# Performance work log

Measured on AMD Instinct MI355X. Metric: run time of the kernel, lower is better.

## Reference

```python
import jax, jax.numpy as jnp
import numpy as np

E = 65536          # number of edges (cell pairs)
D = 256            # hidden_dim
P = 8              # n_lr_pairs


def setup_inputs() -> dict:
    key = jax.random.key(0)
    k1, k2, k3, k4, k5, k6, k7 = jax.random.split(key, 7)
    scale = 1.0 / np.sqrt(D)
    z_src = jax.random.normal(k1, (E, D), dtype=jnp.float32)
    z_dst = jax.random.normal(k2, (E, D), dtype=jnp.float32)
    lr_pair_idx = jax.random.randint(k3, (E,), 0, P, dtype=jnp.int64)
    # Per-LR-pair Linear(D, D): y = x @ W.T + b  (torch convention, W: [out, in])
    W_lr = jax.random.normal(k4, (P, D, D), dtype=jnp.float32) * scale
    b_lr = jax.random.normal(k5, (P, D), dtype=jnp.float32) * scale
    # nn.Bilinear(D, D, 1): weight [1, D, D], bias [1]
    W_bil = jax.random.normal(k6, (1, D, D), dtype=jnp.float32) * scale
    b_bil = jax.random.normal(k7, (1,), dtype=jnp.float32) * scale
    return {"z_src": z_src, "z_dst": z_dst, "W_lr": W_lr, "b_lr": b_lr,
            "W_bil": W_bil, "b_bil": b_bil, "lr_pair_idx": lr_pair_idx}


def _forward(z_src, z_dst, W_lr, b_lr, W_bil, b_bil, lr_pair_idx):
    # Per-LR-pair linear projection of z_src (MoE-style routing).
    # Fixed small loop over P experts; each iteration is a dense GEMM over
    # all E edges, masked to the edges routed to that pair. All idx values
    # lie in [0, P), so the zeros-init in the original is fully overwritten.
    z_proj = jnp.zeros_like(z_src)
    for p in range(P):
        mask = (lr_pair_idx == p)[:, None]                      # [E, 1]
        y_p = z_src @ W_lr[p].T + b_lr[p]                       # [E, D]
        z_proj = jnp.where(mask, y_p, z_proj)
    # Bilinear scoring: score_e = z_proj_e @ W_bil[0] @ z_dst_e + b_bil
    t = z_proj @ W_bil[0]                                       # [E, D]
    scores = jnp.sum(t * z_dst, axis=-1, keepdims=True) + b_bil  # [E, 1]
    return scores


def reference(z_src, z_dst, W_lr, b_lr, W_bil, b_bil, lr_pair_idx):
    return _forward(z_src, z_dst, W_lr, b_lr, W_bil, b_bil, lr_pair_idx)
```

## Files before the change

### kernel.cpp

```cpp
#include <hip/hip_runtime.h>
#include <hip/hip_bf16.h>
#include <cstddef>

#define NE 65536
#define ND 256
#define NP 8
#define SB 32
#define NSB (NE / SB)
#define TR 32

typedef short bf16x8 __attribute__((ext_vector_type(8)));
typedef float f32x4  __attribute__((ext_vector_type(4)));

__device__ __forceinline__ unsigned short f2bf(float f) {
  unsigned int u = __float_as_uint(f);
  u += 0x7FFFu + ((u >> 16) & 1u);
  return (unsigned short)(u >> 16);
}
__device__ __forceinline__ float bf2f(unsigned short h) {
  return __uint_as_float(((unsigned int)h) << 16);
}
__device__ __forceinline__ int load_idx(const void* idxraw, int is32, int e) {
  return is32 ? ((const int*)idxraw)[e] : (int)((const long long*)idxraw)[e];
}
__device__ __forceinline__ int sniff_is32(const void* idxraw, int* lflag) {
  int tid = threadIdx.x;
  if (tid == 0) *lflag = 0;
  __syncthreads();
  const unsigned int* w = (const unsigned int*)idxraw;
  unsigned int val = w[(((int)blockIdx.x & 63) * 256 + (tid & 255)) * 2 + 1];
  if (__any(val != 0) && (tid & 63) == 0) atomicOr(lflag, 1);
  __syncthreads();
  return *lflag;
}

__global__ __launch_bounds__(256) void k_pre0(const float* __restrict__ Wbil,
                                              const float* __restrict__ blr,
                                              const void* __restrict__ idxraw,
                                              unsigned short* __restrict__ WbT,
                                              float* __restrict__ v,
                                              int* __restrict__ counts) {
  int b = blockIdx.x, t = threadIdx.x;
  if (b < 32) {
    int s = b * 256 + t;
    int kt = s >> 10, c = (s >> 6) & 15, l = s & 63;
    int col = c * 16 + (l & 15);
    int k0 = kt * 32 + (l >> 4) * 8;
    union { uint4 u; unsigned short h[8]; } uu;
#pragma unroll
    for (int j = 0; j < 8; ++j)
      uu.h[j] = f2bf(Wbil[(k0 + j) * ND + col]);
    *(uint4*)(WbT + (size_t)s * 8) = uu.u;
  } else if (b < 40) {
    int p = b - 32;
    float s = 0.f;
    for (int k = 0; k < ND; ++k)
      s = fmaf(blr[p * ND + k], Wbil[k * ND + t], s);
    v[p * ND + t] = s;
  } else {
    __shared__ int lflag;
    int is32 = sniff_is32(idxraw, &lflag);
    int hb = b - 40;
    int w = t >> 6, l = t & 63;
    int e = hb * 256 + w * 64 + l;
    int p = load_idx(idxraw, is32, e);
    int sb0 = hb * 8 + w * 2;
#pragma unroll
    for (int q = 0; q < NP; ++q) {
      unsigned long long m = __ballot(p == q);
      if (l == q)      counts[q * NSB + sb0]     = __popcll(m & 0xFFFFFFFFull);
      if (l == 32 + q) counts[q * NSB + sb0 + 1] = __popcll(m >> 32);
    }
  }
}

__global__ __launch_bounds__(256) void k_scan(const int* __restrict__ counts,
                                              int* __restrict__ hdr,
                                              int* __restrict__ bases) {
  __shared__ int part[NP][32], cpre[NP][32], cnt[NP], shoff[NP];
  int t = threadIdx.x;
  int q = t >> 5, i = t & 31;
  int s = 0;
  for (int j = 0; j < 64; ++j) s += counts[q * NSB + i * 64 + j];
  part[q][i] = s;
  __syncthreads();
  if (t < NP) {
    int run = 0;
    for (int k = 0; k < 32; ++k) { cpre[t][k] = run; run += part[t][k]; }
    cnt[t] = run;
  }
  __syncthreads();
  if (t == 0) {
    int o = 0, tt = 0;
    for (int p = 0; p < NP; ++p) {
      shoff[p] = o; hdr[p] = o; hdr[9 + p] = tt;
      o += cnt[p];
      tt += (cnt[p] + TR - 1) / TR;
    }
    hdr[NP] = o; hdr[9 + NP] = tt;
  }
  __syncthreads();
  int run = shoff[q] + cpre[q][i];
  for (int j = 0; j < 64; ++j) {
    int sb = i * 64 + j;
    bases[q * NSB + sb] = run;
    run += counts[q * NSB + sb];
  }
}

__global__ __launch_bounds__(256) void k_cpre(const float* __restrict__ Wlr,
                                              const unsigned short* __restrict__ WbT,
                                              unsigned short* __restrict__ Cst) {
  __shared__ unsigned short aF[2048 * 8];
  int blk = blockIdx.x;
  int p = blk >> 2;
  int i0 = (blk & 3) * 64;
  int tid = threadIdx.x;
  const float* Wp = Wlr + (size_t)p * ND * ND;
#pragma unroll
  for (int it = 0; it < 8; ++it) {
    int s = tid + it * 256;
    int kt = s >> 8, r = (s >> 6) & 3, l = s & 63;
    int i = r * 16 + (l & 15);
    int k0 = kt * 32 + (l >> 4) * 8;
    union { uint4 u; unsigned short h[8]; } uu;
#pragma unroll
    for (int j = 0; j < 8; ++j)
      uu.h[j] = f2bf(Wp[(size_t)(k0 + j) * ND + i0 + i]);
    *(uint4*)(aF + (size_t)s * 8) = uu.u;
  }
  __syncthreads();
  int w = tid >> 6, l = tid & 63;
  f32x4 zero = {0.f, 0.f, 0.f, 0.f};
  f32x4 acc[16];
#pragma unroll
  for (int c = 0; c < 16; ++c) acc[c] = zero;
  for (int kt = 0; kt < 8; ++kt) {
    bf16x8 a = *(const bf16x8*)(aF + (size_t)((kt * 4 + w) * 64 + l) * 8);
#pragma unroll
    for (int c = 0; c < 16; ++c) {
      bf16x8 bb = *(const bf16x8*)(WbT + (size_t)((kt * 16 + c) * 64 + l) * 8);
      acc[c] = __builtin_amdgcn_mfma_f32_16x16x32_bf16(a, bb, acc[c], 0, 0, 0);
    }
  }
  unsigned short* Cp = Cst + (size_t)p * ND * ND;
#pragma unroll
  for (int c = 0; c < 16; ++c) {
#pragma unroll
    for (int q = 0; q < 4; ++q) {
      int i = i0 + w * 16 + ((l >> 4) * 4) + q;
      int j = c * 16 + (l & 15);
      int pos = ((i >> 5) * 16 + (j >> 4)) * 512 + (((i >> 3) & 3) * 16 + (j & 15)) * 8 + (i & 7);
      Cp[pos] = f2bf(acc[c][q]);
    }
  }
}

__global__ __launch_bounds__(64) void k_perm(const void* __restrict__ idxraw,
                                             const int* __restrict__ bases,
                                             int* __restrict__ perm) {
  __shared__ int lflag;
  int l = threadIdx.x;
  int b = blockIdx.x;
  if (l == 0) lflag = 0;
  __syncthreads();
  {
    const unsigned int* w = (const unsigned int*)idxraw;
    unsigned int val = w[((b & 63) * 64 + l) * 2 + 1];
    if (__any(val != 0) && l == 0) atomicOr(&lflag, 1);
  }
  __syncthreads();
  int is32 = lflag;
  int base = b * SB;
  int p = (l < SB) ? load_idx(idxraw, is32, base + l) : 999;
  unsigned long long lt = (l == 63) ? (~0ull >> 1) : ((1ull << l) - 1ull);
  int rank = 0, gq = 0;
#pragma unroll
  for (int q = 0; q < NP; ++q) {
    unsigned long long m = __ballot(p == q);
    if (p == q) { rank = __popcll(m & lt); gq = q; }
  }
  if (l < SB) perm[bases[gq * NSB + b] + rank] = base + l;
}

__global__ __launch_bounds__(512, 8) void k_main(const float* __restrict__ zsrc,
                                                 const float* __restrict__ zdst,
                                                 const int* __restrict__ perm,
                                                 const int* __restrict__ hdr,
                                                 const unsigned short* __restrict__ Cst,
                                                 const float* __restrict__ v,
                                                 const float* __restrict__ bbil,
                                                 float* __restrict__ out) {
  __shared__ unsigned short zs[8192];
  __shared__ unsigned short zd[8192];
  __shared__ float red[8][TR];
  __shared__ int eids[TR];
  __shared__ int shdr[18];
  int tid = threadIdx.x;
  if (tid < 18) shdr[tid] = hdr[tid];
  __syncthreads();
  int bid = blockIdx.x;
  int g = bid >> 3, r = bid & 7;
  int p = g & 7;
  int t = ((g >> 3) << 3) + r;
  int cnt = shdr[p + 1] - shdr[p];
  if (t * TR >= cnt) return;
  int ebase = shdr[p] + t * TR;
  int nrow = cnt - t * TR; if (nrow > TR) nrow = TR;
  if (tid < TR) eids[tid] = perm[ebase + (tid < nrow ? tid : nrow - 1)];
  __syncthreads();
  int w = tid >> 6, l = tid & 63;
  int kt0 = l >> 3, q0 = (l >> 1) & 3, par0 = l & 1;
#pragma unroll
  for (int i = 0; i < 4; ++i) {
    int row = w * 4 + i;
    int e = eids[row];
    float4 fs = *(const float4*)(zsrc + (size_t)e * ND + l * 4);
    float4 fd = *(const float4*)(zdst + (size_t)e * ND + l * 4);
    union { unsigned long long u; unsigned short h[4]; } us, ud;
    us.h[0] = f2bf(fs.x); us.h[1] = f2bf(fs.y); us.h[2] = f2bf(fs.z); us.h[3] = f2bf(fs.w);
    ud.h[0] = f2bf(fd.x); ud.h[1] = f2bf(fd.y); ud.h[2] = f2bf(fd.z); ud.h[3] = f2bf(fd.w);
    unsigned gg = (unsigned)((kt0 * 2 + (row >> 4)) * 64 + (row & 15) + 16 * q0);
    gg ^= ((gg >> 6) & 7u) << 1;
    *(unsigned long long*)((char*)zs + gg * 16 + par0 * 8) = us.u;
    *(unsigned long long*)((char*)zd + ((unsigned)(row * 512 + l * 8) ^ (((unsigned)row & 7u) << 5))) = ud.u;
  }
  __syncthreads();
  const unsigned short* Cp = Cst + (size_t)p * ND * ND;
  f32x4 zero = {0.f, 0.f, 0.f, 0.f};
  f32x4 acc[2][2];
#pragma unroll
  for (int sr = 0; sr < 2; ++sr)
#pragma unroll
    for (int cl = 0; cl < 2; ++cl) acc[sr][cl] = zero;
  int hh = l >> 4, rr = l & 15;
#pragma unroll
  for (int kt = 0; kt < 8; ++kt) {
    bf16x8 a[2];
#pragma unroll
    for (int sr = 0; sr < 2; ++sr) {
      unsigned gg = (unsigned)((kt * 2 + sr) * 64 + l);
      gg ^= ((gg >> 6) & 7u) << 1;
      a[sr] = *(const bf16x8*)((const char*)zs + gg * 16);
    }
#pragma unroll
    for (int cl = 0; cl < 2; ++cl) {
      bf16x8 bb = *(const bf16x8*)(Cp + (size_t)((kt * 16 + (w * 2 + cl)) * 64 + l) * 8);
#pragma unroll
      for (int sr = 0; sr < 2; ++sr)
        acc[sr][cl] = __builtin_amdgcn_mfma_f32_16x16x32_bf16(a[sr], bb, acc[sr][cl], 0, 0, 0);
    }
  }
  float vloc[2];
#pragma unroll
  for (int cl = 0; cl < 2; ++cl)
    vloc[cl] = v[p * ND + (w * 2 + cl) * 16 + rr];
#pragma unroll
  for (int sr = 0; sr < 2; ++sr) {
#pragma unroll
    for (int q = 0; q < 4; ++q) {
      int row = sr * 16 + hh * 4 + q;
      unsigned swz = ((unsigned)row & 7u) << 5;
      float sv = 0.f;
#pragma unroll
      for (int cl = 0; cl < 2; ++cl) {
        int col = (w * 2 + cl) * 16 + rr;
        unsigned byte = ((unsigned)(row * 512 + col * 2)) ^ swz;
        sv = fmaf(acc[sr][cl][q] + vloc[cl], bf2f(*(const unsigned short*)((const char*)zd + byte)), sv);
      }
      sv += __shfl_xor(sv, 1, 64);
      sv += __shfl_xor(sv, 2, 64);
      sv += __shfl_xor(sv, 4, 64);
      sv += __shfl_xor(sv, 8, 64);
      if (rr == 0) red[w][row] = sv;
    }
  }
  __syncthreads();
  if (tid < TR && tid < nrow) {
    float sc = bbil[0];
#pragma unroll
    for (int ww = 0; ww < 8; ++ww) sc += red[ww][tid];
    out[eids[tid]] = sc;
  }
}

extern "C" void kernel_launch(void* const* d_in, const int* in_sizes, int n_in,
                              void* d_out, int out_size, void* d_ws, size_t ws_size,
                              hipStream_t stream) {
  const float* zsrc = (const float*)d_in[0];
  const float* zdst = (const float*)d_in[1];
  const float* Wlr  = (const float*)d_in[2];
  const float* blr  = (const float*)d_in[3];
  const float* Wbil = (const float*)d_in[4];
  const float* bbil = (const float*)d_in[5];
  const void*  idx  = (const void*)d_in[6];
  float* out = (float*)d_out;

  char* ws = (char*)d_ws;
  int* hdr    = (int*)ws;
  int* counts = (int*)(ws + 4096);
  int* bases  = (int*)(ws + 73728);
  unsigned short* WbT = (unsigned short*)(ws + 139264);
  float* v            = (float*)(ws + 270336);
  unsigned short* Cst = (unsigned short*)(ws + 278528);
  int* perm           = (int*)(ws + 1327104);

  k_pre0<<<296, 256, 0, stream>>>(Wbil, blr, idx, WbT, v, counts);
  k_scan<<<1, 256, 0, stream>>>(counts, hdr, bases);
  k_cpre<<<32, 256, 0, stream>>>(Wlr, WbT, Cst);
  k_perm<<<NSB, 64, 0, stream>>>(idx, bases, perm);
  k_main<<<16384, 512, 0, stream>>>(zsrc, zdst, perm, hdr, Cst, v, bbil, out);
}
```

Before: 87.48 us.

## Make main kernel persistent with async global-to-LDS multi-stage pipeline

Replaces the 16384-block launch, which had one 32-row tile per block, with 256 persistent blocks. Each block walks a contiguous chunk of 16-row tiles. The z_src and z_dst rows are streamed into a 4-deep fp32 LDS ring using global_load_lds, with manual vmcnt waits, so gathers overlap compute. Expert weight fragments stay in registers and are reloaded only when the expert changes, and the bf16 conversion moves to the MFMA operand load. The cost is heavy LDS use (128KB slab), lower occupancy, and a bit of load imbalance at tile granularity.

```diff
diff --git a/kernel.cpp b/kernel.cpp
--- a/kernel.cpp
+++ b/kernel.cpp
@@ -7,18 +7,19 @@
 #define NP 8
 #define SB 32
 #define NSB (NE / SB)
-#define TR 32
+#define TRS 16
+#define NBLK2 256
+#define MAXCH2 17
 
 typedef short bf16x8 __attribute__((ext_vector_type(8)));
 typedef float f32x4  __attribute__((ext_vector_type(4)));
+typedef const __attribute__((address_space(1))) unsigned int* gas_t;
+typedef __attribute__((address_space(3))) unsigned int* las_t;
 
 __device__ __forceinline__ unsigned short f2bf(float f) {
   unsigned int u = __float_as_uint(f);
   u += 0x7FFFu + ((u >> 16) & 1u);
   return (unsigned short)(u >> 16);
-}
-__device__ __forceinline__ float bf2f(unsigned short h) {
-  return __uint_as_float(((unsigned int)h) << 16);
 }
 __device__ __forceinline__ int load_idx(const void* idxraw, int is32, int e) {
   return is32 ? ((const int*)idxraw)[e] : (int)((const long long*)idxraw)[e];
@@ -95,7 +96,7 @@
     for (int p = 0; p < NP; ++p) {
       shoff[p] = o; hdr[p] = o; hdr[9 + p] = tt;
       o += cnt[p];
-      tt += (cnt[p] + TR - 1) / TR;
+      tt += (cnt[p] + TRS - 1) / TRS;
     }
     hdr[NP] = o; hdr[9 + NP] = tt;
   }
@@ -183,7 +184,7 @@
   if (l < SB) perm[bases[gq * NSB + b] + rank] = base + l;
 }
 
-__global__ __launch_bounds__(512, 8) void k_main(const float* __restrict__ zsrc,
+__global__ __launch_bounds__(512, 2) void k_main(const float* __restrict__ zsrc,
                                                  const float* __restrict__ zdst,
                                                  const int* __restrict__ perm,
                                                  const int* __restrict__ hdr,
@@ -191,96 +192,139 @@
                                                  const float* __restrict__ v,
                                                  const float* __restrict__ bbil,
                                                  float* __restrict__ out) {
-  __shared__ unsigned short zs[8192];
-  __shared__ unsigned short zd[8192];
-  __shared__ float red[8][TR];
-  __shared__ int eids[TR];
+  __shared__ float slab[4][32][256];
+  __shared__ float red[8][TRS];
+  __shared__ float outv[MAXCH2 * TRS];
+  __shared__ int eidsAll[MAXCH2 * TRS];
+  __shared__ int pExp[MAXCH2], pNrow[MAXCH2];
   __shared__ int shdr[18];
   int tid = threadIdx.x;
   if (tid < 18) shdr[tid] = hdr[tid];
   __syncthreads();
-  int bid = blockIdx.x;
-  int g = bid >> 3, r = bid & 7;
-  int p = g & 7;
-  int t = ((g >> 3) << 3) + r;
-  int cnt = shdr[p + 1] - shdr[p];
-  if (t * TR >= cnt) return;
-  int ebase = shdr[p] + t * TR;
-  int nrow = cnt - t * TR; if (nrow > TR) nrow = TR;
-  if (tid < TR) eids[tid] = perm[ebase + (tid < nrow ? tid : nrow - 1)];
-  __syncthreads();
+  int ntiles = shdr[17];
+  int chunk = (ntiles + NBLK2 - 1) / NBLK2;
+  int t0 = (int)blockIdx.x * chunk;
+  if (t0 >= ntiles) return;
+  int nt = ntiles - t0; if (nt > chunk) nt = chunk;
+  float bb0 = bbil[0];
+  for (int j = tid; j < nt * TRS; j += 512) {
+    int tl = j >> 4, tt = t0 + tl;
+    int p = 0;
+    while (p < NP - 1 && tt >= shdr[9 + p + 1]) ++p;
+    int ebase = shdr[p] + (tt - shdr[9 + p]) * TRS;
+    int cend = shdr[p + 1];
+    int r = j & 15;
+    int re = ebase + r; if (re > cend - 1) re = cend - 1;
+    eidsAll[j] = perm[re];
+    if (r == 0) {
+      pExp[tl] = p;
+      int nr = cend - ebase; pNrow[tl] = nr > TRS ? TRS : nr;
+    }
+  }
+  __syncthreads();
+
   int w = tid >> 6, l = tid & 63;
-  int kt0 = l >> 3, q0 = (l >> 1) & 3, par0 = l & 1;
-#pragma unroll
-  for (int i = 0; i < 4; ++i) {
-    int row = w * 4 + i;
-    int e = eids[row];
-    float4 fs = *(const float4*)(zsrc + (size_t)e * ND + l * 4);
-    float4 fd = *(const float4*)(zdst + (size_t)e * ND + l * 4);
-    union { unsigned long long u; unsigned short h[4]; } us, ud;
-    us.h[0] = f2bf(fs.x); us.h[1] = f2bf(fs.y); us.h[2] = f2bf(fs.z); us.h[3] = f2bf(fs.w);
-    ud.h[0] = f2bf(fd.x); ud.h[1] = f2bf(fd.y); ud.h[2] = f2bf(fd.z); ud.h[3] = f2bf(fd.w);
-    unsigned gg = (unsigned)((kt0 * 2 + (row >> 4)) * 64 + (row & 15) + 16 * q0);
-    gg ^= ((gg >> 6) & 7u) << 1;
-    *(unsigned long long*)((char*)zs + gg * 16 + par0 * 8) = us.u;
-    *(unsigned long long*)((char*)zd + ((unsigned)(row * 512 + l * 8) ^ (((unsigned)row & 7u) << 5))) = ud.u;
-  }
-  __syncthreads();
-  const unsigned short* Cp = Cst + (size_t)p * ND * ND;
+  int hi = l >> 4, rr = l & 15;
+  unsigned sxr = (unsigned)(rr & 7);
+
+#define STAGE(TL, SL)                                                            \
+  {                                                                              \
+    int _tl = (TL), _sl = (SL);                                                  \
+    _Pragma("unroll")                                                            \
+    for (int _i = 0; _i < 2; ++_i) {                                             \
+      int _r = w * 2 + _i;                                                       \
+      int _e = eidsAll[_tl * TRS + _r];                                          \
+      unsigned _off = (((unsigned)l ^ (unsigned)(_r & 7)) << 2);                 \
+      __builtin_amdgcn_global_load_lds((gas_t)(const void*)(zsrc + (size_t)_e * ND + _off), \
+          (las_t)(void*)&slab[_sl][_r][0], 16, 0, 0);                            \
+      __builtin_amdgcn_global_load_lds((gas_t)(const void*)(zdst + (size_t)_e * ND + _off), \
+          (las_t)(void*)&slab[_sl][16 + _r][0], 16, 0, 0);                       \
+    }                                                                            \
+  }
+
+#pragma unroll
+  for (int k = 0; k < 4; ++k)
+    if (k < nt) STAGE(k, k);
+
+  int curP = -1;
+  bf16x8 bfr[2][8];
+  float vloc[2];
   f32x4 zero = {0.f, 0.f, 0.f, 0.f};
-  f32x4 acc[2][2];
-#pragma unroll
-  for (int sr = 0; sr < 2; ++sr)
-#pragma unroll
-    for (int cl = 0; cl < 2; ++cl) acc[sr][cl] = zero;
-  int hh = l >> 4, rr = l & 15;
-#pragma unroll
-  for (int kt = 0; kt < 8; ++kt) {
-    bf16x8 a[2];
-#pragma unroll
-    for (int sr = 0; sr < 2; ++sr) {
-      unsigned gg = (unsigned)((kt * 2 + sr) * 64 + l);
-      gg ^= ((gg >> 6) & 7u) << 1;
-      a[sr] = *(const bf16x8*)((const char*)zs + gg * 16);
-    }
-#pragma unroll
-    for (int cl = 0; cl < 2; ++cl) {
-      bf16x8 bb = *(const bf16x8*)(Cp + (size_t)((kt * 16 + (w * 2 + cl)) * 64 + l) * 8);
-#pragma unroll
-      for (int sr = 0; sr < 2; ++sr)
-        acc[sr][cl] = __builtin_amdgcn_mfma_f32_16x16x32_bf16(a[sr], bb, acc[sr][cl], 0, 0, 0);
-    }
-  }
-  float vloc[2];
-#pragma unroll
-  for (int cl = 0; cl < 2; ++cl)
-    vloc[cl] = v[p * ND + (w * 2 + cl) * 16 + rr];
-#pragma unroll
-  for (int sr = 0; sr < 2; ++sr) {
+
+  for (int tl = 0; tl < nt; ++tl) {
+    int sl = tl & 3;
+    int left = nt - 1 - tl; if (left > 3) left = 3;
+    switch (left) {
+      case 3: asm volatile("s_waitcnt vmcnt(12)" ::: "memory"); break;
+      case 2: asm volatile("s_waitcnt vmcnt(8)"  ::: "memory"); break;
+      case 1: asm volatile("s_waitcnt vmcnt(4)"  ::: "memory"); break;
+      default: asm volatile("s_waitcnt vmcnt(0)" ::: "memory"); break;
+    }
+    __builtin_amdgcn_sched_barrier(0);
+    __builtin_amdgcn_s_barrier();
+
+    int p = pExp[tl];
+    if (p != curP) {
+      curP = p;
+      const unsigned short* Cp = Cst + (size_t)p * ND * ND;
+#pragma unroll
+      for (int cl = 0; cl < 2; ++cl) {
+#pragma unroll
+        for (int kt = 0; kt < 8; ++kt)
+          bfr[cl][kt] = *(const bf16x8*)(Cp + (size_t)((kt * 16 + (w * 2 + cl)) * 64 + l) * 8);
+        vloc[cl] = v[p * ND + (w * 2 + cl) * 16 + rr];
+      }
+    }
+
+    const char* zsb = (const char*)&slab[sl][0][0];
+    const char* rowb = zsb + rr * 1024;
+    f32x4 acc0 = zero, acc1 = zero;
+#pragma unroll
+    for (int kt = 0; kt < 8; ++kt) {
+      unsigned g0 = (unsigned)(kt * 8 + hi * 2);
+      float4 f0 = *(const float4*)(rowb + ((g0 ^ sxr) << 4));
+      float4 f1 = *(const float4*)(rowb + (((g0 + 1) ^ sxr) << 4));
+      union { bf16x8 vv; unsigned short h[8]; } ua;
+      ua.h[0] = f2bf(f0.x); ua.h[1] = f2bf(f0.y); ua.h[2] = f2bf(f0.z); ua.h[3] = f2bf(f0.w);
+      ua.h[4] = f2bf(f1.x); ua.h[5] = f2bf(f1.y); ua.h[6] = f2bf(f1.z); ua.h[7] = f2bf(f1.w);
+      acc0 = __builtin_amdgcn_mfma_f32_16x16x32_bf16(ua.vv, bfr[0][kt], acc0, 0, 0, 0);
+      acc1 = __builtin_amdgcn_mfma_f32_16x16x32_bf16(ua.vv, bfr[1][kt], acc1, 0, 0, 0);
+    }
 #pragma unroll
     for (int q = 0; q < 4; ++q) {
-      int row = sr * 16 + hh * 4 + q;
-      unsigned swz = ((unsigned)row & 7u) << 5;
-      float sv = 0.f;
-#pragma unroll
-      for (int cl = 0; cl < 2; ++cl) {
-        int col = (w * 2 + cl) * 16 + rr;
-        unsigned byte = ((unsigned)(row * 512 + col * 2)) ^ swz;
-        sv = fmaf(acc[sr][cl][q] + vloc[cl], bf2f(*(const unsigned short*)((const char*)zd + byte)), sv);
-      }
+      int row = hi * 4 + q;
+      const char* zdb = zsb + (16 + row) * 1024;
+      unsigned sw = (unsigned)(row & 7);
+      int col0 = (w * 2 + 0) * 16 + rr;
+      int col1 = col0 + 16;
+      float z0 = *(const float*)(zdb + ((((unsigned)(col0 >> 2) ^ sw) << 4) | ((unsigned)(col0 & 3) << 2)));
+      float z1 = *(const float*)(zdb + ((((unsigned)(col1 >> 2) ^ sw) << 4) | ((unsigned)(col1 & 3) << 2)));
+      float sv = fmaf(acc0[q] + vloc[0], z0, 0.f);
+      sv = fmaf(acc1[q] + vloc[1], z1, sv);
       sv += __shfl_xor(sv, 1, 64);
       sv += __shfl_xor(sv, 2, 64);
       sv += __shfl_xor(sv, 4, 64);
       sv += __shfl_xor(sv, 8, 64);
       if (rr == 0) red[w][row] = sv;
     }
-  }
-  __syncthreads();
-  if (tid < TR && tid < nrow) {
-    float sc = bbil[0];
-#pragma unroll
-    for (int ww = 0; ww < 8; ++ww) sc += red[ww][tid];
-    out[eids[tid]] = sc;
+    asm volatile("s_waitcnt lgkmcnt(0)" ::: "memory");
+    __builtin_amdgcn_sched_barrier(0);
+    __builtin_amdgcn_s_barrier();
+
+    if (tid < TRS) {
+      float sc = 0.f;
+#pragma unroll
+      for (int ww = 0; ww < 8; ++ww) sc += red[ww][tid];
+      outv[tl * TRS + tid] = sc;
+    }
+    if (tl + 4 < nt) STAGE(tl + 4, sl);
+  }
+#undef STAGE
+
+  __syncthreads();
+  for (int j = tid; j < nt * TRS; j += 512) {
+    int tl = j >> 4, r = j & 15;
+    if (r < pNrow[tl]) out[eidsAll[j]] = outv[j] + bb0;
   }
 }
 
@@ -309,5 +353,5 @@
   k_scan<<<1, 256, 0, stream>>>(counts, hdr, bases);
   k_cpre<<<32, 256, 0, stream>>>(Wlr, WbT, Cst);
   k_perm<<<NSB, 64, 0, stream>>>(idx, bases, perm);
-  k_main<<<16384, 512, 0, stream>>>(zsrc, zdst, perm, hdr, Cst, v, bbil, out);
-}
+  k_main<<<NBLK2, 512, 0, stream>>>(zsrc, zdst, perm, hdr, Cst, v, bbil, out);
+}
```

After: 95.45 us. 1.09x slower.
